# Performance work log

Hardware: AMD Instinct MI355X
Metric: run time of the kernel (lower is better)

## Reference

```python
import jax, jax.numpy as jnp
import numpy as np

H = 16      # num_heads
D = 64      # hidden_size per head
IN = 1024   # input_size = H*D
B, S = 4, 2048

def setup_inputs() -> dict:
    key = jax.random.key(0)
    ks = jax.random.split(key, 5)
    scale = 1.0 / np.sqrt(IN)
    return {
        "x": jax.random.normal(ks[0], (B, S, IN), dtype=jnp.float32),
        "Wq": jax.random.normal(ks[1], (IN, H * D), dtype=jnp.float32) * scale,
        "bq": jnp.zeros((H * D,), dtype=jnp.float32),
        "Wk": jax.random.normal(ks[2], (IN, H * D), dtype=jnp.float32) * scale,
        "bk": jnp.zeros((H * D,), dtype=jnp.float32),
        "Wv": jax.random.normal(ks[3], (IN, H * D), dtype=jnp.float32) * scale,
        "bv": jnp.zeros((H * D,), dtype=jnp.float32),
        "Wo": jax.random.normal(ks[4], (H * D, IN), dtype=jnp.float32) * scale,
        "bo": jnp.zeros((IN,), dtype=jnp.float32),
    }

def reference(x, Wq, bq, Wk, bk, Wv, bv, Wo, bo):
    b, s, _ = x.shape
    # projections -> [b, h, s, d]
    def split_heads(t):
        return t.reshape(b, s, H, D).transpose(0, 2, 1, 3)
    q = split_heads(x @ Wq + bq)
    k = split_heads(x @ Wk + bk)
    v = split_heads(x @ Wv + bv)
    scores = jnp.einsum('bhqd,bhkd->bhqk', q, k) / jnp.sqrt(jnp.float32(D))
    probs = jax.nn.softmax(scores, axis=-1)            # [b,h,s,s]
    attn = jnp.einsum('bhqk,bhkd->bhqd', probs, v)     # [b,h,s,d]
    attn = attn.transpose(0, 2, 1, 3).reshape(b, s, H * D)
    out = attn @ Wo + bo
    return out, jnp.mean(probs, axis=1)
```

## Files before the change

kernel.cpp:

```cpp
#include <hip/hip_runtime.h>

typedef __attribute__((ext_vector_type(8))) short s8v;
typedef __attribute__((ext_vector_type(4))) short s4v;
typedef __attribute__((ext_vector_type(4))) float f4v;

#define DEV __device__ __forceinline__

DEV short b16(float f) {
  unsigned u = __builtin_bit_cast(unsigned, f);
  u = (u + 0x7fffu + ((u >> 16) & 1u)) >> 16;
  return (short)u;
}

DEV unsigned pk2(float a, float b) {
#if __has_builtin(__builtin_amdgcn_cvt_pk_bf16_f32)
  auto p = __builtin_amdgcn_cvt_pk_bf16_f32(a, b);
  return __builtin_bit_cast(unsigned, p);
#else
  return (unsigned)(unsigned short)b16(a) | ((unsigned)(unsigned short)b16(b) << 16);
#endif
}

DEV float fexp2(float x) {
#if __has_builtin(__builtin_amdgcn_exp2f)
  return __builtin_amdgcn_exp2f(x);
#else
  return exp2f(x);
#endif
}

DEV void gl_lds16(const short* g, short* l) {
  __builtin_amdgcn_global_load_lds((const __attribute__((address_space(1))) void*)g,
                                   (__attribute__((address_space(3))) void*)l, 16, 0, 0);
}

__global__ __launch_bounds__(256) void cast_f32_bf16(const float* __restrict__ in,
                                                     short* __restrict__ out, int n4) {
  int i = blockIdx.x * 256 + threadIdx.x;
  if (i >= n4) return;
  float4 v = ((const float4*)in)[i];
  s4v o; o.x = b16(v.x); o.y = b16(v.y); o.z = b16(v.z); o.w = b16(v.w);
  ((s4v*)out)[i] = o;
}

__global__ __launch_bounds__(256) void wtrans(const float* __restrict__ W, short* __restrict__ Wt) {
  int id = blockIdx.x * 256 + threadIdx.x;
  int k8 = id >> 10;
  int n  = id & 1023;
  s8v o;
#pragma unroll
  for (int j = 0; j < 8; ++j) o[j] = b16(W[(k8 * 8 + j) * 1024 + n]);
  *(s8v*)&Wt[n * 1024 + k8 * 8] = o;
}

template <bool OUT_BF16>
__global__ __launch_bounds__(256) void gemm128(const short* __restrict__ A,
                                               const short* __restrict__ Bt,
                                               const float* __restrict__ bias,
                                               void* __restrict__ Cout) {
  __shared__ short As[128 * 64];
  __shared__ short Bs[128 * 64];
  const int tid = threadIdx.x;
  const int w = tid >> 6, lane = tid & 63, quad = lane >> 4, l15 = lane & 15;
  const int wm = w >> 1, wn = w & 1;
  const int m0 = blockIdx.y * 128, n0 = blockIdx.x * 128;
  const int lr = lane >> 3, lc = (lane & 7) * 8;
  f4v acc[4][4] = {};
  for (int k0 = 0; k0 < 1024; k0 += 64) {
#pragma unroll
    for (int i = 0; i < 4; ++i) {
      int c = i * 4 + w;
      int r = c * 8 + lr;
      gl_lds16(&A[(m0 + r) * 1024 + k0 + lc], &As[c * 512]);
      gl_lds16(&Bt[(n0 + r) * 1024 + k0 + lc], &Bs[c * 512]);
    }
    __syncthreads();
#pragma unroll
    for (int kk = 0; kk < 2; ++kk) {
      s8v af[4], bf[4];
#pragma unroll
      for (int mt = 0; mt < 4; ++mt) af[mt] = *(const s8v*)&As[(wm * 64 + mt * 16 + l15) * 64 + kk * 32 + quad * 8];
#pragma unroll
      for (int nt = 0; nt < 4; ++nt) bf[nt] = *(const s8v*)&Bs[(wn * 64 + nt * 16 + l15) * 64 + kk * 32 + quad * 8];
#pragma unroll
      for (int mt = 0; mt < 4; ++mt)
#pragma unroll
        for (int nt = 0; nt < 4; ++nt)
          acc[mt][nt] = __builtin_amdgcn_mfma_f32_16x16x32_bf16(af[mt], bf[nt], acc[mt][nt], 0, 0, 0);
    }
    __syncthreads();
  }
#pragma unroll
  for (int nt = 0; nt < 4; ++nt) {
    const int col = n0 + wn * 64 + nt * 16 + l15;
    const float bcol = bias[col];
#pragma unroll
    for (int mt = 0; mt < 4; ++mt)
#pragma unroll
      for (int r = 0; r < 4; ++r) {
        const int row = m0 + wm * 64 + mt * 16 + quad * 4 + r;
        float v = acc[mt][nt][r] + bcol;
        if (OUT_BF16) ((short*)Cout)[row * 1024 + col] = b16(v);
        else          ((float*)Cout)[row * 1024 + col] = v;
      }
  }
}

__global__ __launch_bounds__(256) void vtrans(const short* __restrict__ V, short* __restrict__ Vt) {
  __shared__ short T[128][72];
  const int st = blockIdx.x, h = blockIdx.y, b = blockIdx.z;
  const int tid = threadIdx.x;
#pragma unroll
  for (int i = 0; i < 4; ++i) {
    int c = tid + i * 256;
    int r = c >> 3, c8 = (c & 7) * 8;
    *(s8v*)&T[r][c8] = *(const s8v*)&V[((b * 2048 + st * 128 + r) * 16 + h) * 64 + c8];
  }
  __syncthreads();
#pragma unroll
  for (int i = 0; i < 4; ++i) {
    int id = tid + i * 256;
    int d = id & 63, s8 = id >> 6;
    s8v o;
#pragma unroll
    for (int j = 0; j < 8; ++j) o[j] = T[s8 * 8 + j][d];
    *(s8v*)&Vt[((b * 16 + h) * 64 + d) * 2048 + st * 128 + s8 * 8] = o;
  }
}

__global__ __launch_bounds__(256, 3) void attn_ctx(const short* __restrict__ Q, const short* __restrict__ K,
                                                   const short* __restrict__ Vt,
                                                   float* __restrict__ rbuf, short* __restrict__ ctx) {
  __shared__ __align__(16) char smem[50432];
  short* Ks = (short*)smem;
  short* Vs = (short*)(smem + 16384);
  short* Ps = (short*)(smem + 32768);
  short* Qs = Ps;
  float* l_part = (float*)(smem + 49152);
  float* l_s    = (float*)(smem + 50176);
  const int q64 = blockIdx.x, h = blockIdx.y, b = blockIdx.z;
  const int tid = threadIdx.x, w = tid >> 6, lane = tid & 63, quad = lane >> 4, l15 = lane & 15;
  const int bh = b * 16 + h, q0 = q64 * 64;
  const float C2 = 0.18033688011f;

#pragma unroll
  for (int i = 0; i < 2; ++i) {
    int c = tid + i * 256;
    int r = c >> 3, cc = c & 7;
    *(s8v*)&Qs[r * 64 + (((cc ^ (r & 7))) << 3)] =
        *(const s8v*)&Q[((b * 2048 + q0 + r) * 16 + h) * 64 + cc * 8];
  }
  __syncthreads();
  s8v qf[4][2];
#pragma unroll
  for (int nt = 0; nt < 4; ++nt) {
    int r = nt * 16 + l15;
    qf[nt][0] = *(const s8v*)&Qs[r * 64 + ((quad ^ (r & 7)) << 3)];
    qf[nt][1] = *(const s8v*)&Qs[r * 64 + (((4 + quad) ^ (r & 7)) << 3)];
  }
  const short* kbase = &K[((long)(b * 2048) * 16 + h) * 64];
  const short* vbase = &Vt[(long)(bh * 64) * 2048];
  f4v o[4] = {};
  float l_acc[4] = {0.f, 0.f, 0.f, 0.f};

  for (int kt = 0; kt < 16; ++kt) {
    __syncthreads();
#pragma unroll
    for (int i = 0; i < 4; ++i) {
      int c = tid + i * 256;
      int r = c >> 3, cc = c & 7;
      *(s8v*)&Ks[r * 64 + ((cc ^ (r & 7)) << 3)] =
          *(const s8v*)&kbase[(kt * 128 + r) * 1024 + cc * 8];
    }
#pragma unroll
    for (int i = 0; i < 4; ++i) {
      int c = tid + i * 256;
      int d = c >> 4, ck = c & 15;
      *(s8v*)&Vs[d * 128 + ((ck ^ (d & 15)) << 3)] =
          *(const s8v*)&vbase[d * 2048 + kt * 128 + ck * 8];
    }
    __syncthreads();
#pragma unroll
    for (int mt = 0; mt < 2; ++mt) {
      int kr = w * 32 + mt * 16 + l15;
      s8v a0 = *(const s8v*)&Ks[kr * 64 + ((quad ^ (kr & 7)) << 3)];
      s8v a1 = *(const s8v*)&Ks[kr * 64 + (((4 + quad) ^ (kr & 7)) << 3)];
#pragma unroll
      for (int nt = 0; nt < 4; ++nt) {
        f4v st = {};
        st = __builtin_amdgcn_mfma_f32_16x16x32_bf16(a0, qf[nt][0], st, 0, 0, 0);
        st = __builtin_amdgcn_mfma_f32_16x16x32_bf16(a1, qf[nt][1], st, 0, 0, 0);
        float e0 = fexp2(st[0] * C2), e1 = fexp2(st[1] * C2);
        float e2 = fexp2(st[2] * C2), e3 = fexp2(st[3] * C2);
        l_acc[nt] += (e0 + e1) + (e2 + e3);
        uint2 pp; pp.x = pk2(e0, e1); pp.y = pk2(e2, e3);
        int q = nt * 16 + l15;
        int chunk = (w * 4 + mt * 2 + (quad >> 1)) ^ l15;
        *(uint2*)&Ps[q * 128 + (chunk << 3) + (quad & 1) * 4] = pp;
      }
    }
    __syncthreads();
#pragma unroll
    for (int kk = 0; kk < 4; ++kk) {
      int qr = w * 16 + l15;
      s8v a = *(const s8v*)&Ps[qr * 128 + (((kk * 4 + quad) ^ (qr & 15)) << 3)];
#pragma unroll
      for (int dt = 0; dt < 4; ++dt) {
        int d = dt * 16 + l15;
        s8v vb = *(const s8v*)&Vs[d * 128 + (((kk * 4 + quad) ^ (d & 15)) << 3)];
        o[dt] = __builtin_amdgcn_mfma_f32_16x16x32_bf16(a, vb, o[dt], 0, 0, 0);
      }
    }
  }

#pragma unroll
  for (int nt = 0; nt < 4; ++nt) {
    float v = l_acc[nt];
    v += __shfl_xor(v, 16, 64);
    v += __shfl_xor(v, 32, 64);
    if (quad == 0) l_part[w * 64 + nt * 16 + l15] = v;
  }
  __syncthreads();
  if (tid < 64) {
    float s = l_part[tid] + l_part[64 + tid] + l_part[128 + tid] + l_part[192 + tid];
    float rv = 1.0f / s;
    l_s[tid] = rv;
    rbuf[bh * 2048 + q0 + tid] = rv;
  }
  __syncthreads();
  float rvq[4];
#pragma unroll
  for (int r = 0; r < 4; ++r) rvq[r] = l_s[w * 16 + quad * 4 + r];
#pragma unroll
  for (int dt = 0; dt < 4; ++dt)
#pragma unroll
    for (int r = 0; r < 4; ++r) {
      int sq = q0 + w * 16 + quad * 4 + r;
      ctx[((b * 2048 + sq) * 16 + h) * 64 + dt * 16 + l15] = b16(o[dt][r] * rvq[r]);
    }
}

__global__ __launch_bounds__(256) void mean_probs(const short* __restrict__ Q, const short* __restrict__ K,
                                                  const float* __restrict__ rbuf, float* __restrict__ outm) {
  __shared__ short Qs[128][72];
  __shared__ short Ks[128][72];
  __shared__ float r_s[128];
  const int k128 = blockIdx.x, q128 = blockIdx.y, b = blockIdx.z;
  const int tid = threadIdx.x, w = tid >> 6, lane = tid & 63, quad = lane >> 4, l15 = lane & 15;
  f4v mn[2][8] = {};
  const float C2 = 0.18033688011f;
  for (int h = 0; h < 16; ++h) {
    __syncthreads();
#pragma unroll
    for (int i = 0; i < 4; ++i) {
      int c = tid + i * 256;
      int r = c >> 3, c8 = (c & 7) * 8;
      *(s8v*)&Qs[r][c8] = *(const s8v*)&Q[((b * 2048 + q128 * 128 + r) * 16 + h) * 64 + c8];
      *(s8v*)&Ks[r][c8] = *(const s8v*)&K[((b * 2048 + k128 * 128 + r) * 16 + h) * 64 + c8];
    }
    if (tid < 128) r_s[tid] = rbuf[(b * 16 + h) * 2048 + q128 * 128 + tid] * 0.0625f;
    __syncthreads();
    s8v aq[2][2];
#pragma unroll
    for (int qt = 0; qt < 2; ++qt) {
      aq[qt][0] = *(const s8v*)&Qs[w * 32 + qt * 16 + l15][quad * 8];
      aq[qt][1] = *(const s8v*)&Qs[w * 32 + qt * 16 + l15][32 + quad * 8];
    }
    float rr[2][4];
#pragma unroll
    for (int qt = 0; qt < 2; ++qt)
#pragma unroll
      for (int r = 0; r < 4; ++r) rr[qt][r] = r_s[w * 32 + qt * 16 + quad * 4 + r];
#pragma unroll
    for (int ktile = 0; ktile < 8; ++ktile) {
      s8v b0 = *(const s8v*)&Ks[ktile * 16 + l15][quad * 8];
      s8v b1 = *(const s8v*)&Ks[ktile * 16 + l15][32 + quad * 8];
#pragma unroll
      for (int qt = 0; qt < 2; ++qt) {
        f4v sc = {};
        sc = __builtin_amdgcn_mfma_f32_16x16x32_bf16(aq[qt][0], b0, sc, 0, 0, 0);
        sc = __builtin_amdgcn_mfma_f32_16x16x32_bf16(aq[qt][1], b1, sc, 0, 0, 0);
#pragma unroll
        for (int r = 0; r < 4; ++r)
          mn[qt][ktile][r] += fexp2(sc[r] * C2) * rr[qt][r];
      }
    }
  }
#pragma unroll
  for (int qt = 0; qt < 2; ++qt)
#pragma unroll
    for (int ktile = 0; ktile < 8; ++ktile)
#pragma unroll
      for (int r = 0; r < 4; ++r) {
        long qrow = q128 * 128 + w * 32 + qt * 16 + quad * 4 + r;
        outm[((long)b * 2048 + qrow) * 2048 + k128 * 128 + ktile * 16 + l15] = mn[qt][ktile][r];
      }
}

extern "C" void kernel_launch(void* const* d_in, const int* in_sizes, int n_in,
                              void* d_out, int out_size, void* d_ws, size_t ws_size,
                              hipStream_t stream) {
  (void)in_sizes; (void)n_in; (void)out_size; (void)ws_size;
  const float* x  = (const float*)d_in[0];
  const float* Wq = (const float*)d_in[1];
  const float* bq = (const float*)d_in[2];
  const float* Wk = (const float*)d_in[3];
  const float* bk = (const float*)d_in[4];
  const float* Wv = (const float*)d_in[5];
  const float* bv = (const float*)d_in[6];
  const float* Wo = (const float*)d_in[7];
  const float* bo = (const float*)d_in[8];
  float* out  = (float*)d_out;
  float* outm = out + 8388608;

  char* ws = (char*)d_ws;
  short* xb  = (short*)(ws);
  short* Wqt = (short*)(ws + 16777216);
  short* Wkt = (short*)(ws + 18874368);
  short* Wvt = (short*)(ws + 20971520);
  short* Wot = (short*)(ws + 23068672);
  short* Qb  = (short*)(ws + 25165824);
  short* Kb  = (short*)(ws + 41943040);
  short* Vb  = (short*)(ws + 58720256);
  short* Vt  = (short*)(ws + 75497472);
  float* rbuf = (float*)Vb;
  short* ctx = xb;

  cast_f32_bf16<<<8192, 256, 0, stream>>>(x, xb, 2097152);
  wtrans<<<512, 256, 0, stream>>>(Wq, Wqt);
  wtrans<<<512, 256, 0, stream>>>(Wk, Wkt);
  wtrans<<<512, 256, 0, stream>>>(Wv, Wvt);
  wtrans<<<512, 256, 0, stream>>>(Wo, Wot);
  dim3 gg(8, 64);
  gemm128<true><<<gg, 256, 0, stream>>>(xb, Wqt, bq, Qb);
  gemm128<true><<<gg, 256, 0, stream>>>(xb, Wkt, bk, Kb);
  gemm128<true><<<gg, 256, 0, stream>>>(xb, Wvt, bv, Vb);
  vtrans<<<dim3(16, 16, 4), 256, 0, stream>>>(Vb, Vt);
  attn_ctx<<<dim3(32, 16, 4), 256, 0, stream>>>(Qb, Kb, Vt, rbuf, ctx);
  mean_probs<<<dim3(16, 16, 4), 256, 0, stream>>>(Qb, Kb, rbuf, outm);
  gemm128<false><<<gg, 256, 0, stream>>>(ctx, Wot, bo, out);
}
```

Measured before the change: 462.0 us.

## Fold softmax scale into Q projection and load K/V tiles via direct-to-LDS

Pre-multiplies the Q projection output by the log2e/sqrt(D) constant in the GEMM epilogue, so the attention and mean-probs kernels can call exp2 on raw scores without a per-element multiply. Replaces register-staged global-to-LDS copies of K, V, Q tiles in attn_ctx and mean_probs with gl_lds16 direct loads, using XOR-swizzled source addresses so the LDS layout keeps its bank-conflict-free pattern. mean_probs switches from padded to swizzled shared arrays to match. Rounding Q to bf16 after scaling slightly changes numerics.

```diff
diff --git a/kernel.cpp b/kernel.cpp
--- a/kernel.cpp
+++ b/kernel.cpp
@@ -57,7 +57,7 @@
 __global__ __launch_bounds__(256) void gemm128(const short* __restrict__ A,
                                                const short* __restrict__ Bt,
                                                const float* __restrict__ bias,
-                                               void* __restrict__ Cout) {
+                                               void* __restrict__ Cout, float scale) {
   __shared__ short As[128 * 64];
   __shared__ short Bs[128 * 64];
   const int tid = threadIdx.x;
@@ -99,7 +99,7 @@
 #pragma unroll
       for (int r = 0; r < 4; ++r) {
         const int row = m0 + wm * 64 + mt * 16 + quad * 4 + r;
-        float v = acc[mt][nt][r] + bcol;
+        float v = (acc[mt][nt][r] + bcol) * scale;
         if (OUT_BF16) ((short*)Cout)[row * 1024 + col] = b16(v);
         else          ((float*)Cout)[row * 1024 + col] = v;
       }
@@ -141,7 +141,6 @@
   const int q64 = blockIdx.x, h = blockIdx.y, b = blockIdx.z;
   const int tid = threadIdx.x, w = tid >> 6, lane = tid & 63, quad = lane >> 4, l15 = lane & 15;
   const int bh = b * 16 + h, q0 = q64 * 64;
-  const float C2 = 0.18033688011f;
 
 #pragma unroll
   for (int i = 0; i < 2; ++i) {
@@ -160,6 +159,10 @@
   }
   const short* kbase = &K[((long)(b * 2048) * 16 + h) * 64];
   const short* vbase = &Vt[(long)(bh * 64) * 2048];
+  const int krow = w * 8 + (lane >> 3);
+  const short* ksrc = kbase + krow * 1024 + (((lane & 7) ^ (lane >> 3)) << 3);
+  const int vrow = w * 4 + (lane >> 4);
+  const short* vsrc = vbase + vrow * 2048 + (((lane & 15) ^ vrow) << 3);
   f4v o[4] = {};
   float l_acc[4] = {0.f, 0.f, 0.f, 0.f};
 
@@ -167,17 +170,8 @@
     __syncthreads();
 #pragma unroll
     for (int i = 0; i < 4; ++i) {
-      int c = tid + i * 256;
-      int r = c >> 3, cc = c & 7;
-      *(s8v*)&Ks[r * 64 + ((cc ^ (r & 7)) << 3)] =
-          *(const s8v*)&kbase[(kt * 128 + r) * 1024 + cc * 8];
-    }
-#pragma unroll
-    for (int i = 0; i < 4; ++i) {
-      int c = tid + i * 256;
-      int d = c >> 4, ck = c & 15;
-      *(s8v*)&Vs[d * 128 + ((ck ^ (d & 15)) << 3)] =
-          *(const s8v*)&vbase[d * 2048 + kt * 128 + ck * 8];
+      gl_lds16(ksrc + kt * 131072 + i * 32768, &Ks[(i * 4 + w) * 512]);
+      gl_lds16(vsrc + kt * 128 + i * 32768, &Vs[(i * 4 + w) * 512]);
     }
     __syncthreads();
 #pragma unroll
@@ -190,8 +184,8 @@
         f4v st = {};
         st = __builtin_amdgcn_mfma_f32_16x16x32_bf16(a0, qf[nt][0], st, 0, 0, 0);
         st = __builtin_amdgcn_mfma_f32_16x16x32_bf16(a1, qf[nt][1], st, 0, 0, 0);
-        float e0 = fexp2(st[0] * C2), e1 = fexp2(st[1] * C2);
-        float e2 = fexp2(st[2] * C2), e3 = fexp2(st[3] * C2);
+        float e0 = fexp2(st[0]), e1 = fexp2(st[1]);
+        float e2 = fexp2(st[2]), e3 = fexp2(st[3]);
         l_acc[nt] += (e0 + e1) + (e2 + e3);
         uint2 pp; pp.x = pk2(e0, e1); pp.y = pk2(e2, e3);
         int q = nt * 16 + l15;
@@ -242,29 +236,31 @@
 
 __global__ __launch_bounds__(256) void mean_probs(const short* __restrict__ Q, const short* __restrict__ K,
                                                   const float* __restrict__ rbuf, float* __restrict__ outm) {
-  __shared__ short Qs[128][72];
-  __shared__ short Ks[128][72];
+  __shared__ __align__(16) short Qs[8192];
+  __shared__ __align__(16) short Ks[8192];
   __shared__ float r_s[128];
   const int k128 = blockIdx.x, q128 = blockIdx.y, b = blockIdx.z;
   const int tid = threadIdx.x, w = tid >> 6, lane = tid & 63, quad = lane >> 4, l15 = lane & 15;
   f4v mn[2][8] = {};
-  const float C2 = 0.18033688011f;
+  const int mrow = w * 8 + (lane >> 3);
+  const int mck8 = ((lane & 7) ^ (lane >> 3)) << 3;
+  const short* qsrc = Q + ((long)(b * 2048 + q128 * 128 + mrow) * 16) * 64 + mck8;
+  const short* ksrc = K + ((long)(b * 2048 + k128 * 128 + mrow) * 16) * 64 + mck8;
   for (int h = 0; h < 16; ++h) {
     __syncthreads();
 #pragma unroll
     for (int i = 0; i < 4; ++i) {
-      int c = tid + i * 256;
-      int r = c >> 3, c8 = (c & 7) * 8;
-      *(s8v*)&Qs[r][c8] = *(const s8v*)&Q[((b * 2048 + q128 * 128 + r) * 16 + h) * 64 + c8];
-      *(s8v*)&Ks[r][c8] = *(const s8v*)&K[((b * 2048 + k128 * 128 + r) * 16 + h) * 64 + c8];
+      gl_lds16(qsrc + h * 64 + i * 32768, &Qs[(i * 4 + w) * 512]);
+      gl_lds16(ksrc + h * 64 + i * 32768, &Ks[(i * 4 + w) * 512]);
     }
     if (tid < 128) r_s[tid] = rbuf[(b * 16 + h) * 2048 + q128 * 128 + tid] * 0.0625f;
     __syncthreads();
     s8v aq[2][2];
 #pragma unroll
     for (int qt = 0; qt < 2; ++qt) {
-      aq[qt][0] = *(const s8v*)&Qs[w * 32 + qt * 16 + l15][quad * 8];
-      aq[qt][1] = *(const s8v*)&Qs[w * 32 + qt * 16 + l15][32 + quad * 8];
+      int r = w * 32 + qt * 16 + l15;
+      aq[qt][0] = *(const s8v*)&Qs[r * 64 + ((quad ^ (r & 7)) << 3)];
+      aq[qt][1] = *(const s8v*)&Qs[r * 64 + (((4 + quad) ^ (r & 7)) << 3)];
     }
     float rr[2][4];
 #pragma unroll
@@ -273,8 +269,9 @@
       for (int r = 0; r < 4; ++r) rr[qt][r] = r_s[w * 32 + qt * 16 + quad * 4 + r];
 #pragma unroll
     for (int ktile = 0; ktile < 8; ++ktile) {
-      s8v b0 = *(const s8v*)&Ks[ktile * 16 + l15][quad * 8];
-      s8v b1 = *(const s8v*)&Ks[ktile * 16 + l15][32 + quad * 8];
+      int kr = ktile * 16 + l15;
+      s8v b0 = *(const s8v*)&Ks[kr * 64 + ((quad ^ (kr & 7)) << 3)];
+      s8v b1 = *(const s8v*)&Ks[kr * 64 + (((4 + quad) ^ (kr & 7)) << 3)];
 #pragma unroll
       for (int qt = 0; qt < 2; ++qt) {
         f4v sc = {};
@@ -282,7 +279,7 @@
         sc = __builtin_amdgcn_mfma_f32_16x16x32_bf16(aq[qt][1], b1, sc, 0, 0, 0);
 #pragma unroll
         for (int r = 0; r < 4; ++r)
-          mn[qt][ktile][r] += fexp2(sc[r] * C2) * rr[qt][r];
+          mn[qt][ktile][r] += fexp2(sc[r]) * rr[qt][r];
       }
     }
   }
@@ -326,17 +323,19 @@
   float* rbuf = (float*)Vb;
   short* ctx = xb;
 
+  const float C2 = 0.18033688011112042f;
+
   cast_f32_bf16<<<8192, 256, 0, stream>>>(x, xb, 2097152);
   wtrans<<<512, 256, 0, stream>>>(Wq, Wqt);
   wtrans<<<512, 256, 0, stream>>>(Wk, Wkt);
   wtrans<<<512, 256, 0, stream>>>(Wv, Wvt);
   wtrans<<<512, 256, 0, stream>>>(Wo, Wot);
   dim3 gg(8, 64);
-  gemm128<true><<<gg, 256, 0, stream>>>(xb, Wqt, bq, Qb);
-  gemm128<true><<<gg, 256, 0, stream>>>(xb, Wkt, bk, Kb);
-  gemm128<true><<<gg, 256, 0, stream>>>(xb, Wvt, bv, Vb);
+  gemm128<true><<<gg, 256, 0, stream>>>(xb, Wqt, bq, Qb, C2);
+  gemm128<true><<<gg, 256, 0, stream>>>(xb, Wkt, bk, Kb, 1.0f);
+  gemm128<true><<<gg, 256, 0, stream>>>(xb, Wvt, bv, Vb, 1.0f);
   vtrans<<<dim3(16, 16, 4), 256, 0, stream>>>(Vb, Vt);
   attn_ctx<<<dim3(32, 16, 4), 256, 0, stream>>>(Qb, Kb, Vt, rbuf, ctx);
   mean_probs<<<dim3(16, 16, 4), 256, 0, stream>>>(Qb, Kb, rbuf, outm);
-  gemm128<false><<<gg, 256, 0, stream>>>(ctx, Wot, bo, out);
-}
+  gemm128<false><<<gg, 256, 0, stream>>>(ctx, Wot, bo, out, 1.0f);
+}
```

New measurement: 445.4 us. 3.6% less time.
